# Performance work log

Measured on AMD Instinct MI355X. Metric: run time of the kernel, lower is better.

The kernel has to match this reference:

```python
import jax, jax.numpy as jnp
import numpy as np


def setup_inputs() -> dict:
    key = jax.random.key(0)
    ks = jax.random.split(key, 5)
    B, S, D = 2, 2048, 1024
    std = 0.02
    return {
        "x": jax.random.normal(ks[0], (B, S, D), dtype=jnp.float32),
        "Wq": jax.random.normal(ks[1], (D, D), dtype=jnp.float32) * std,
        "Wk": jax.random.normal(ks[2], (D, D), dtype=jnp.float32) * std,
        "Wv": jax.random.normal(ks[3], (D, D), dtype=jnp.float32) * std,
        "Wo": jax.random.normal(ks[4], (D, D), dtype=jnp.float32) * std,
        "num_heads": 16,
        "window_size": 512,
    }


def reference(x, Wq, Wk, Wv, Wo, num_heads, window_size):
    B, S, D = x.shape
    H = num_heads
    d = D // H
    scale = d ** (-0.5)

    # QKV projections (torch Linear: y = x @ W.T), split heads -> b h s d
    def proj(W):
        return (x @ W.T).reshape(B, S, H, d).transpose(0, 2, 1, 3)

    q, k, v = proj(Wq), proj(Wk), proj(Wv)

    # [B, H, S, S] scores (faithful to the dense SDPA fallback)
    scores = jnp.einsum("bhsd,bhtd->bhst", q, k) * scale

    # sliding-window causal mask: col <= row and row - col < window_size
    pos = jnp.arange(S)
    row, col = pos[:, None], pos[None, :]
    mask = (col <= row) & (row - col < window_size)  # [S, S]
    scores = jnp.where(mask[None, None], scores, -jnp.inf)

    attn = jax.nn.softmax(scores, axis=-1)
    out = jnp.einsum("bhst,bhtd->bhsd", attn, v)  # b h s d
    out = out.transpose(0, 2, 1, 3).reshape(B, S, D)  # merge heads
    return out @ Wo.T
```

## Files before the change

### kernel.cpp

```cpp
#include <hip/hip_runtime.h>
#include <cstdint>

typedef uint16_t u16;
typedef __attribute__((ext_vector_type(8))) short short8;
typedef __attribute__((ext_vector_type(4))) float f32x4;

__device__ __forceinline__ u16 f2bf(float f) {
  uint32_t u = __float_as_uint(f);
  u += 0x7fff + ((u >> 16) & 1);
  return (u16)(u >> 16);
}
__device__ __forceinline__ uint32_t pk2bf(float a, float b) {
  uint32_t ua = __float_as_uint(a) + 0x8000u;
  uint32_t ub = __float_as_uint(b) + 0x8000u;
  return (ua >> 16) | (ub & 0xFFFF0000u);
}

#define GLL16(gp, lp) __builtin_amdgcn_global_load_lds( \
    (__attribute__((address_space(1))) void*)(gp), \
    (__attribute__((address_space(3))) void*)(lp), 16, 0, 0)

#define SBAR()       __builtin_amdgcn_s_barrier()
#define WAIT_LGKM0() asm volatile("s_waitcnt lgkmcnt(0)" ::: "memory")
#define WAIT_VM(N)   asm volatile("s_waitcnt vmcnt(" #N ")" ::: "memory")
#define MEMBAR()     asm volatile("" ::: "memory")

__global__ void cvt_all(const float* __restrict__ x,  const float* __restrict__ wq,
                        const float* __restrict__ wk, const float* __restrict__ wv,
                        const float* __restrict__ wo,
                        u16* __restrict__ xb, u16* __restrict__ wcat, u16* __restrict__ wob) {
  int i = blockIdx.x * 256 + threadIdx.x;
  const float4* src; ushort4* dst; int off; float sc = 1.0f;
  if (i < 1048576)      { src = (const float4*)x;  dst = (ushort4*)xb;              off = i; }
  else if (i < 1310720) { src = (const float4*)wq; dst = (ushort4*)wcat;            off = i - 1048576;
                          sc = 0.18033688011112042f; }
  else if (i < 1572864) { src = (const float4*)wk; dst = (ushort4*)wcat + 262144;   off = i - 1310720; }
  else if (i < 1835008) { src = (const float4*)wv; dst = (ushort4*)wcat + 524288;   off = i - 1572864; }
  else                  { src = (const float4*)wo; dst = (ushort4*)wob;             off = i - 1835008; }
  float4 v = src[off];
  ushort4 o;
  o.x = f2bf(v.x * sc); o.y = f2bf(v.y * sc); o.z = f2bf(v.z * sc); o.w = f2bf(v.w * sc);
  dst[off] = o;
}

template<int OUT_BF16>
__global__ __launch_bounds__(256, 2) void gemm128(const u16* __restrict__ A,
                                                  const u16* __restrict__ B,
                                                  void* __restrict__ Cout,
                                                  int N, int K, int ntN) {
  __shared__ u16 sm[2][2][128 * 64];
  const int tid  = threadIdx.x;
  const int lane = tid & 63, w = tid >> 6;
  const int wr = w >> 1, wc = w & 1;
  const int g = lane >> 4, lr = lane & 15;

  const int cpx = gridDim.x >> 3;
  const int id  = blockIdx.x;
  const int sw  = (id & 7) * cpx + (id >> 3);
  const int row0 = (sw / ntN) * 128, col0 = (sw % ntN) * 128;
  const int T = K >> 6;

  f32x4 acc[4][4];
  #pragma unroll
  for (int i = 0; i < 4; ++i)
    #pragma unroll
    for (int j = 0; j < 4; ++j) acc[i][j] = (f32x4){0.f, 0.f, 0.f, 0.f};

  auto STAGE = [&](int kt, int bufi) {
    #pragma unroll
    for (int ab = 0; ab < 2; ++ab) {
      const u16* __restrict__ src = ab ? B : A;
      const int rb = ab ? col0 : row0;
      #pragma unroll
      for (int j = 0; j < 4; ++j) {
        int r  = j * 32 + w * 8 + (lane >> 3);
        int sb = ((lane & 7) << 4) ^ ((r & 7) << 4);
        const u16* gp = src + (size_t)(rb + r) * K + kt * 64 + (sb >> 1);
        GLL16(gp, &sm[bufi][ab][(size_t)(j * 32 + w * 8) * 64]);
      }
    }
  };

  STAGE(0, 0); STAGE(1, 1);
  WAIT_VM(8); SBAR(); MEMBAR();

  for (int t = 0; t < T; ++t) {
    const int cur = t & 1;
    short8 a[4][2], b[4][2];
    #pragma unroll
    for (int mm = 0; mm < 4; ++mm)
      #pragma unroll
      for (int kh = 0; kh < 2; ++kh) {
        int row = wr * 64 + mm * 16 + lr;
        int col = (kh * 64 + g * 16) ^ ((row & 7) << 4);
        a[mm][kh] = *(const short8*)((const char*)&sm[cur][0][0] + row * 128 + col);
      }
    #pragma unroll
    for (int nn = 0; nn < 4; ++nn)
      #pragma unroll
      for (int kh = 0; kh < 2; ++kh) {
        int row = wc * 64 + nn * 16 + lr;
        int col = (kh * 64 + g * 16) ^ ((row & 7) << 4);
        b[nn][kh] = *(const short8*)((const char*)&sm[cur][1][0] + row * 128 + col);
      }
    WAIT_LGKM0(); MEMBAR(); SBAR(); MEMBAR();

    if (t + 2 < T) STAGE(t + 2, cur);

    __builtin_amdgcn_s_setprio(1);
    #pragma unroll
    for (int kh = 0; kh < 2; ++kh)
      #pragma unroll
      for (int mm = 0; mm < 4; ++mm)
        #pragma unroll
        for (int nn = 0; nn < 4; ++nn)
          acc[mm][nn] = __builtin_amdgcn_mfma_f32_16x16x32_bf16(
              a[mm][kh], b[nn][kh], acc[mm][nn], 0, 0, 0);
    __builtin_amdgcn_s_setprio(0);

    if (t + 1 < T) {
      if (t + 2 < T) { WAIT_VM(8); } else { WAIT_VM(0); }
      SBAR(); MEMBAR();
    }
  }

  #pragma unroll
  for (int i = 0; i < 4; ++i)
    #pragma unroll
    for (int j = 0; j < 4; ++j)
      #pragma unroll
      for (int ri = 0; ri < 4; ++ri) {
        int rr = row0 + wr * 64 + i * 16 + g * 4 + ri;
        int cc = col0 + wc * 64 + j * 16 + lr;
        if (OUT_BF16) ((u16*)Cout)[(size_t)rr * N + cc] = f2bf(acc[i][j][ri]);
        else          ((float*)Cout)[(size_t)rr * N + cc] = acc[i][j][ri];
      }
}

__global__ __launch_bounds__(256) void attn_swa(const u16* __restrict__ QKV, u16* __restrict__ O) {
  const int S = 2048;
  const int qb = blockIdx.x * 64;
  const int b = blockIdx.y >> 4, h = blockIdx.y & 15;
  const int tid = threadIdx.x;
  const int lane = tid & 63, w = tid >> 6;
  const int g = lane >> 4, lr = lane & 15;

  __shared__ u16 Klds[2][64 * 64];
  __shared__ u16 Vt[64][72];
  __shared__ u16 Plds[4][16][72];

  const u16* Qb = QKV + (size_t)b * S * 3072 + h * 64;
  const u16* Kb = QKV + (size_t)b * S * 3072 + 1024 + h * 64;
  const u16* Vb = QKV + (size_t)b * S * 3072 + 2048 + h * 64;

  const int qw = qb + w * 16;
  short8 qf0 = *(const short8*)(Qb + (size_t)(qw + lr) * 3072 + g * 8);
  short8 qf1 = *(const short8*)(Qb + (size_t)(qw + lr) * 3072 + 32 + g * 8);

  float ls = 0.f;
  f32x4 accO[4];
  #pragma unroll
  for (int i = 0; i < 4; ++i) accO[i] = (f32x4){0.f, 0.f, 0.f, 0.f};

  int ks = qb - 511; if (ks < 0) ks = 0; ks &= ~63;
  const int ke = qb + 63;
  const int nt = ((ke - ks) >> 6) + 1;

  short8 vreg0, vreg1;

  auto STAGE_K = [&](int kb, int buf) {
    #pragma unroll
    for (int c = 0; c < 2; ++c) {
      int r  = c * 32 + w * 8 + (lane >> 3);
      int sb = ((lane & 7) << 4) ^ ((r & 7) << 4);
      const u16* gp = Kb + (size_t)(kb + r) * 3072 + (sb >> 1);
      u16* lp = Klds[buf] + c * 2048 + w * 512;
      GLL16(gp, lp);
    }
  };
  auto LOAD_V = [&](int kb) {
    vreg0 = *(const short8*)(Vb + (size_t)(kb + lane) * 3072 + w * 8);
    vreg1 = *(const short8*)(Vb + (size_t)(kb + lane) * 3072 + w * 8 + 32);
  };
  auto WRITE_V = [&]() {
    #pragma unroll
    for (int j = 0; j < 8; ++j) Vt[w * 8 + j][lane]      = (u16)vreg0[j];
    #pragma unroll
    for (int j = 0; j < 8; ++j) Vt[w * 8 + 32 + j][lane] = (u16)vreg1[j];
  };

  STAGE_K(ks, 0);
  LOAD_V(ks);
  __syncthreads();
  WRITE_V();
  __syncthreads();

  int cur = 0, kb = ks;
  for (int t = 0; t < nt; ++t, kb += 64) {
    const int nxt = cur ^ 1;
    const bool more = (t + 1 < nt);
    if (more) { STAGE_K(kb + 64, nxt); LOAD_V(kb + 64); }

    float p[4][4];
    #pragma unroll
    for (int st = 0; st < 4; ++st) {
      f32x4 c4 = (f32x4){0.f, 0.f, 0.f, 0.f};
      int r = st * 16 + lr;
      int swz = (r & 7) << 4;
      const char* krow = (const char*)(Klds[cur]) + r * 128;
      short8 kf0 = *(const short8*)(krow + ((g * 16) ^ swz));
      short8 kf1 = *(const short8*)(krow + ((64 + g * 16) ^ swz));
      __builtin_amdgcn_s_setprio(1);
      c4 = __builtin_amdgcn_mfma_f32_16x16x32_bf16(kf0, qf0, c4, 0, 0, 0);
      c4 = __builtin_amdgcn_mfma_f32_16x16x32_bf16(kf1, qf1, c4, 0, 0, 0);
      __builtin_amdgcn_s_setprio(0);
      #pragma unroll
      for (int ri = 0; ri < 4; ++ri) p[st][ri] = c4[ri];
    }

    const bool clean = (kb + 63 <= qw) && (qw + 15 - kb < 512);
    if (clean) {
      #pragma unroll
      for (int st = 0; st < 4; ++st)
        #pragma unroll
        for (int ri = 0; ri < 4; ++ri)
          p[st][ri] = __builtin_amdgcn_exp2f(p[st][ri]);
    } else {
      const int base = qw + lr - kb;
      #pragma unroll
      for (int st = 0; st < 4; ++st)
        #pragma unroll
        for (int ri = 0; ri < 4; ++ri) {
          float e = __builtin_amdgcn_exp2f(p[st][ri]);
          p[st][ri] = ((uint32_t)(base - (st * 16 + g * 4 + ri)) < 512u) ? e : 0.f;
        }
    }

    {
      float s = 0.f;
      #pragma unroll
      for (int st = 0; st < 4; ++st)
        #pragma unroll
        for (int ri = 0; ri < 4; ++ri) s += p[st][ri];
      s += __shfl_xor(s, 16);
      s += __shfl_xor(s, 32);
      ls += s;
    }

    #pragma unroll
    for (int st = 0; st < 4; ++st) {
      uint2 u2;
      u2.x = pk2bf(p[st][0], p[st][1]);
      u2.y = pk2bf(p[st][2], p[st][3]);
      *(uint2*)(&Plds[w][lr][st * 16 + g * 4]) = u2;
    }

    short8 pf0 = *(const short8*)(&Plds[w][lr][g * 8]);
    short8 pf1 = *(const short8*)(&Plds[w][lr][32 + g * 8]);
    __builtin_amdgcn_s_setprio(1);
    #pragma unroll
    for (int dt = 0; dt < 4; ++dt) {
      short8 vf0 = *(const short8*)(&Vt[dt * 16 + lr][g * 8]);
      short8 vf1 = *(const short8*)(&Vt[dt * 16 + lr][32 + g * 8]);
      accO[dt] = __builtin_amdgcn_mfma_f32_16x16x32_bf16(pf0, vf0, accO[dt], 0, 0, 0);
      accO[dt] = __builtin_amdgcn_mfma_f32_16x16x32_bf16(pf1, vf1, accO[dt], 0, 0, 0);
    }
    __builtin_amdgcn_s_setprio(0);

    __syncthreads();
    if (more) WRITE_V();
    __syncthreads();
    cur = nxt;
  }

  float lsq[4];
  #pragma unroll
  for (int ri = 0; ri < 4; ++ri) lsq[ri] = __shfl(ls, g * 4 + ri);
  #pragma unroll
  for (int dt = 0; dt < 4; ++dt)
    #pragma unroll
    for (int ri = 0; ri < 4; ++ri) {
      int qi = qw + g * 4 + ri;
      O[(size_t)(b * S + qi) * 1024 + h * 64 + dt * 16 + lr] = f2bf(accO[dt][ri] / lsq[ri]);
    }
}

extern "C" void kernel_launch(void* const* d_in, const int* in_sizes, int n_in,
                              void* d_out, int out_size, void* d_ws, size_t ws_size,
                              hipStream_t stream) {
  const float* x  = (const float*)d_in[0];
  const float* Wq = (const float*)d_in[1];
  const float* Wk = (const float*)d_in[2];
  const float* Wv = (const float*)d_in[3];
  const float* Wo = (const float*)d_in[4];

  char* ws = (char*)d_ws;
  u16* xb   = (u16*)(ws);
  u16* Wcat = (u16*)(ws + (8  << 20));
  u16* Wob  = (u16*)(ws + (14 << 20));
  u16* QKV  = (u16*)(ws + (16 << 20));
  u16* Oatt = (u16*)(ws + (40 << 20));

  cvt_all<<<8192, 256, 0, stream>>>(x, Wq, Wk, Wv, Wo, xb, Wcat, Wob);
  gemm128<1><<<768, 256, 0, stream>>>(xb, Wcat, QKV, 3072, 1024, 24);
  attn_swa<<<dim3(32, 32), 256, 0, stream>>>(QKV, Oatt);
  gemm128<0><<<256, 256, 0, stream>>>(Oatt, Wob, d_out, 1024, 1024, 8);
}
```

Measured before the change: 94.51 us.

## Process 128 queries per attention block, two 16-row query groups per wave

Doubles the query tile per attention block from 64 to 128 rows, so each wave handles two 16-row query groups that share every K/V tile loaded into LDS. This halves the grid and the number of K/V loads per query, and raises the ratio of MFMA work to LDS traffic. The cost is more registers per thread and fewer blocks (512 on the GPU), which may reduce occupancy and load balance. The tile range also widens, so more masked work is done per block.

```diff
diff --git a/kernel.cpp b/kernel.cpp
--- a/kernel.cpp
+++ b/kernel.cpp
@@ -139,7 +139,7 @@
 
 __global__ __launch_bounds__(256) void attn_swa(const u16* __restrict__ QKV, u16* __restrict__ O) {
   const int S = 2048;
-  const int qb = blockIdx.x * 64;
+  const int qb = blockIdx.x * 128;
   const int b = blockIdx.y >> 4, h = blockIdx.y & 15;
   const int tid = threadIdx.x;
   const int lane = tid & 63, w = tid >> 6;
@@ -147,23 +147,29 @@
 
   __shared__ u16 Klds[2][64 * 64];
   __shared__ u16 Vt[64][72];
-  __shared__ u16 Plds[4][16][72];
+  __shared__ u16 Plds[4][32][72];
 
   const u16* Qb = QKV + (size_t)b * S * 3072 + h * 64;
   const u16* Kb = QKV + (size_t)b * S * 3072 + 1024 + h * 64;
   const u16* Vb = QKV + (size_t)b * S * 3072 + 2048 + h * 64;
 
-  const int qw = qb + w * 16;
-  short8 qf0 = *(const short8*)(Qb + (size_t)(qw + lr) * 3072 + g * 8);
-  short8 qf1 = *(const short8*)(Qb + (size_t)(qw + lr) * 3072 + 32 + g * 8);
-
-  float ls = 0.f;
-  f32x4 accO[4];
-  #pragma unroll
-  for (int i = 0; i < 4; ++i) accO[i] = (f32x4){0.f, 0.f, 0.f, 0.f};
+  const int qw = qb + w * 32;
+  short8 qf[2][2];
+  #pragma unroll
+  for (int qg = 0; qg < 2; ++qg)
+    #pragma unroll
+    for (int kh = 0; kh < 2; ++kh)
+      qf[qg][kh] = *(const short8*)(Qb + (size_t)(qw + qg * 16 + lr) * 3072 + kh * 32 + g * 8);
+
+  float ls[2] = {0.f, 0.f};
+  f32x4 accO[2][4];
+  #pragma unroll
+  for (int qg = 0; qg < 2; ++qg)
+    #pragma unroll
+    for (int i = 0; i < 4; ++i) accO[qg][i] = (f32x4){0.f, 0.f, 0.f, 0.f};
 
   int ks = qb - 511; if (ks < 0) ks = 0; ks &= ~63;
-  const int ke = qb + 63;
+  const int ke = qb + 127;
   const int nt = ((ke - ks) >> 6) + 1;
 
   short8 vreg0, vreg1;
@@ -201,69 +207,80 @@
     const bool more = (t + 1 < nt);
     if (more) { STAGE_K(kb + 64, nxt); LOAD_V(kb + 64); }
 
-    float p[4][4];
+    float p[2][4][4];
     #pragma unroll
     for (int st = 0; st < 4; ++st) {
-      f32x4 c4 = (f32x4){0.f, 0.f, 0.f, 0.f};
+      f32x4 c4[2];
+      c4[0] = (f32x4){0.f, 0.f, 0.f, 0.f};
+      c4[1] = (f32x4){0.f, 0.f, 0.f, 0.f};
       int r = st * 16 + lr;
       int swz = (r & 7) << 4;
       const char* krow = (const char*)(Klds[cur]) + r * 128;
       short8 kf0 = *(const short8*)(krow + ((g * 16) ^ swz));
       short8 kf1 = *(const short8*)(krow + ((64 + g * 16) ^ swz));
       __builtin_amdgcn_s_setprio(1);
-      c4 = __builtin_amdgcn_mfma_f32_16x16x32_bf16(kf0, qf0, c4, 0, 0, 0);
-      c4 = __builtin_amdgcn_mfma_f32_16x16x32_bf16(kf1, qf1, c4, 0, 0, 0);
+      c4[0] = __builtin_amdgcn_mfma_f32_16x16x32_bf16(kf0, qf[0][0], c4[0], 0, 0, 0);
+      c4[1] = __builtin_amdgcn_mfma_f32_16x16x32_bf16(kf0, qf[1][0], c4[1], 0, 0, 0);
+      c4[0] = __builtin_amdgcn_mfma_f32_16x16x32_bf16(kf1, qf[0][1], c4[0], 0, 0, 0);
+      c4[1] = __builtin_amdgcn_mfma_f32_16x16x32_bf16(kf1, qf[1][1], c4[1], 0, 0, 0);
       __builtin_amdgcn_s_setprio(0);
       #pragma unroll
-      for (int ri = 0; ri < 4; ++ri) p[st][ri] = c4[ri];
-    }
-
-    const bool clean = (kb + 63 <= qw) && (qw + 15 - kb < 512);
-    if (clean) {
+      for (int ri = 0; ri < 4; ++ri) { p[0][st][ri] = c4[0][ri]; p[1][st][ri] = c4[1][ri]; }
+    }
+
+    #pragma unroll
+    for (int qg = 0; qg < 2; ++qg) {
+      const int q0 = qw + qg * 16;
+      const bool clean = (kb + 63 <= q0) && (q0 + 15 - kb < 512);
+      if (clean) {
+        #pragma unroll
+        for (int st = 0; st < 4; ++st)
+          #pragma unroll
+          for (int ri = 0; ri < 4; ++ri)
+            p[qg][st][ri] = __builtin_amdgcn_exp2f(p[qg][st][ri]);
+      } else {
+        const int base = q0 + lr - kb;
+        #pragma unroll
+        for (int st = 0; st < 4; ++st)
+          #pragma unroll
+          for (int ri = 0; ri < 4; ++ri) {
+            float e = __builtin_amdgcn_exp2f(p[qg][st][ri]);
+            p[qg][st][ri] = ((uint32_t)(base - (st * 16 + g * 4 + ri)) < 512u) ? e : 0.f;
+          }
+      }
+      float s = 0.f;
       #pragma unroll
       for (int st = 0; st < 4; ++st)
         #pragma unroll
-        for (int ri = 0; ri < 4; ++ri)
-          p[st][ri] = __builtin_amdgcn_exp2f(p[st][ri]);
-    } else {
-      const int base = qw + lr - kb;
-      #pragma unroll
-      for (int st = 0; st < 4; ++st)
-        #pragma unroll
-        for (int ri = 0; ri < 4; ++ri) {
-          float e = __builtin_amdgcn_exp2f(p[st][ri]);
-          p[st][ri] = ((uint32_t)(base - (st * 16 + g * 4 + ri)) < 512u) ? e : 0.f;
-        }
-    }
-
-    {
-      float s = 0.f;
-      #pragma unroll
-      for (int st = 0; st < 4; ++st)
-        #pragma unroll
-        for (int ri = 0; ri < 4; ++ri) s += p[st][ri];
+        for (int ri = 0; ri < 4; ++ri) s += p[qg][st][ri];
       s += __shfl_xor(s, 16);
       s += __shfl_xor(s, 32);
-      ls += s;
-    }
-
-    #pragma unroll
-    for (int st = 0; st < 4; ++st) {
-      uint2 u2;
-      u2.x = pk2bf(p[st][0], p[st][1]);
-      u2.y = pk2bf(p[st][2], p[st][3]);
-      *(uint2*)(&Plds[w][lr][st * 16 + g * 4]) = u2;
-    }
-
-    short8 pf0 = *(const short8*)(&Plds[w][lr][g * 8]);
-    short8 pf1 = *(const short8*)(&Plds[w][lr][32 + g * 8]);
+      ls[qg] += s;
+
+      #pragma unroll
+      for (int st = 0; st < 4; ++st) {
+        uint2 u2;
+        u2.x = pk2bf(p[qg][st][0], p[qg][st][1]);
+        u2.y = pk2bf(p[qg][st][2], p[qg][st][3]);
+        *(uint2*)(&Plds[w][qg * 16 + lr][st * 16 + g * 4]) = u2;
+      }
+    }
+
+    short8 pf[2][2];
+    #pragma unroll
+    for (int qg = 0; qg < 2; ++qg) {
+      pf[qg][0] = *(const short8*)(&Plds[w][qg * 16 + lr][g * 8]);
+      pf[qg][1] = *(const short8*)(&Plds[w][qg * 16 + lr][32 + g * 8]);
+    }
     __builtin_amdgcn_s_setprio(1);
     #pragma unroll
     for (int dt = 0; dt < 4; ++dt) {
       short8 vf0 = *(const short8*)(&Vt[dt * 16 + lr][g * 8]);
       short8 vf1 = *(const short8*)(&Vt[dt * 16 + lr][32 + g * 8]);
-      accO[dt] = __builtin_amdgcn_mfma_f32_16x16x32_bf16(pf0, vf0, accO[dt], 0, 0, 0);
-      accO[dt] = __builtin_amdgcn_mfma_f32_16x16x32_bf16(pf1, vf1, accO[dt], 0, 0, 0);
+      accO[0][dt] = __builtin_amdgcn_mfma_f32_16x16x32_bf16(pf[0][0], vf0, accO[0][dt], 0, 0, 0);
+      accO[1][dt] = __builtin_amdgcn_mfma_f32_16x16x32_bf16(pf[1][0], vf0, accO[1][dt], 0, 0, 0);
+      accO[0][dt] = __builtin_amdgcn_mfma_f32_16x16x32_bf16(pf[0][1], vf1, accO[0][dt], 0, 0, 0);
+      accO[1][dt] = __builtin_amdgcn_mfma_f32_16x16x32_bf16(pf[1][1], vf1, accO[1][dt], 0, 0, 0);
     }
     __builtin_amdgcn_s_setprio(0);
 
@@ -273,16 +290,19 @@
     cur = nxt;
   }
 
-  float lsq[4];
-  #pragma unroll
-  for (int ri = 0; ri < 4; ++ri) lsq[ri] = __shfl(ls, g * 4 + ri);
-  #pragma unroll
-  for (int dt = 0; dt < 4; ++dt)
-    #pragma unroll
-    for (int ri = 0; ri < 4; ++ri) {
-      int qi = qw + g * 4 + ri;
-      O[(size_t)(b * S + qi) * 1024 + h * 64 + dt * 16 + lr] = f2bf(accO[dt][ri] / lsq[ri]);
-    }
+  #pragma unroll
+  for (int qg = 0; qg < 2; ++qg) {
+    float lsq[4];
+    #pragma unroll
+    for (int ri = 0; ri < 4; ++ri) lsq[ri] = __shfl(ls[qg], g * 4 + ri);
+    #pragma unroll
+    for (int dt = 0; dt < 4; ++dt)
+      #pragma unroll
+      for (int ri = 0; ri < 4; ++ri) {
+        int qi = qw + qg * 16 + g * 4 + ri;
+        O[(size_t)(b * S + qi) * 1024 + h * 64 + dt * 16 + lr] = f2bf(accO[qg][dt][ri] / lsq[ri]);
+      }
+  }
 }
 
 extern "C" void kernel_launch(void* const* d_in, const int* in_sizes, int n_in,
@@ -303,6 +323,6 @@
 
   cvt_all<<<8192, 256, 0, stream>>>(x, Wq, Wk, Wv, Wo, xb, Wcat, Wob);
   gemm128<1><<<768, 256, 0, stream>>>(xb, Wcat, QKV, 3072, 1024, 24);
-  attn_swa<<<dim3(32, 32), 256, 0, stream>>>(QKV, Oatt);
+  attn_swa<<<dim3(16, 32), 256, 0, stream>>>(QKV, Oatt);
   gemm128<0><<<256, 256, 0, stream>>>(Oatt, Wob, d_out, 1024, 1024, 8);
 }
```

After: 91.01 us. -3.7%, faster.
